# Kernel tuning notes

Hardware: AMD Instinct MI355X
Metric: run time of the kernel (lower is better)

## Reference

```python
import jax, jax.numpy as jnp
import numpy as np

B, S, D, H, E = 2, 2048, 1024, 4096, 8


def setup_inputs() -> dict:
    key = jax.random.key(0)
    k0, k1, k2, k3 = jax.random.split(key, 4)
    x = jax.random.normal(k0, (B, S, D), dtype=jnp.float32)
    router_w = jax.random.normal(k1, (E, D), dtype=jnp.float32) * 0.02   # Top2Router Linear weight [E, D]
    w1 = jax.random.normal(k2, (E, D, H), dtype=jnp.float32) * 0.02      # stacked fc1 weights (transposed: x @ w1[e])
    w2 = jax.random.normal(k3, (E, H, D), dtype=jnp.float32) * 0.02      # stacked fc2 weights
    return {"x": x, "router_w": router_w, "w1": w1, "w2": w2}


def reference(x, router_w, w1, w2):
    # x: [B, S, D] -> flatten tokens. Single-rank EP: all-to-all is identity,
    # microbatch split is a pure overlap trick, per-token math unchanged.
    b, s, d = x.shape
    e = router_w.shape[0]
    xf = x.reshape(-1, d)                                     # [T, D]
    # Top-2 router with renormalized gate weights
    probs = jax.nn.softmax(xf @ router_w.T, axis=-1)          # [T, E]
    topv, topi = jax.lax.top_k(probs, 2)                      # [T, 2]
    topv = topv / (topv.sum(axis=-1, keepdims=True) + 1e-9)
    # Combine weights per expert: cw[t,e] = sum_k topv[t,k] * [topi[t,k]==e]
    cw = (jax.nn.one_hot(topi, e, dtype=xf.dtype) * topv[..., None]).sum(axis=1)  # [T, E]
    # Expert MLPs (dense-over-experts reference for the grouped GEMM)
    h = jax.nn.gelu(jnp.einsum('td,edh->teh', xf, w1), approximate=False)  # [T, E, H]
    y = jnp.einsum('teh,ehd->ted', h, w2)                                   # [T, E, D]
    out = jnp.einsum('te,ted->td', cw, y)                                   # weighted combine (scatter-add equiv.)
    return out.reshape(b, s, d)
```

## Files before the change

### kernel.cpp

```cpp
#include <hip/hip_runtime.h>

#define T_TOK 4096
#define DIM   1024
#define HID   4096
#define NEXP  8
#define MAXROWS 9216

typedef unsigned short u16;
typedef __attribute__((ext_vector_type(8))) short short8;
typedef __attribute__((ext_vector_type(4))) float f32x4;
typedef __attribute__((ext_vector_type(4))) unsigned short u16x4;
typedef __attribute__((ext_vector_type(8))) unsigned short u16x8;

typedef __attribute__((address_space(3))) unsigned int lds_uint;
typedef const __attribute__((address_space(1))) unsigned int gbl_uint;

__device__ __forceinline__ u16 f2bf(float f) {
    union { float f; unsigned int u; } v; v.f = f;
    unsigned int r = v.u + 0x7fffu + ((v.u >> 16) & 1u);
    return (u16)(r >> 16);
}

__device__ __forceinline__ float gelu_f(float v) {
    float u = 1.5957691216f * (v + 0.044715f * v * v * v);
    float s = 1.0f / (1.0f + __expf(-u));
    return v * s;
}

__global__ __launch_bounds__(256)
void transpose_cast(const float* __restrict__ in, u16* __restrict__ out, int R, int C) {
    __shared__ u16 t[64 * 68];
    size_t mo = (size_t)blockIdx.z * R * C;
    const float* ip = in + mo;
    u16* op = out + mo;
    int c0 = blockIdx.x * 64, r0 = blockIdx.y * 64;
    int tid = threadIdx.x;
#pragma unroll
    for (int j = 0; j < 4; ++j) {
        int id = tid + 256 * j;
        int r = id >> 4, cc = id & 15;
        f32x4 v = *(const f32x4*)(ip + (size_t)(r0 + r) * C + c0 + 4 * cc);
        u16x4 w; w.x = f2bf(v.x); w.y = f2bf(v.y); w.z = f2bf(v.z); w.w = f2bf(v.w);
        *(u16x4*)(t + r * 68 + 4 * cc) = w;
    }
    __syncthreads();
#pragma unroll
    for (int j = 0; j < 4; ++j) {
        int id = tid + 256 * j;
        int c = id >> 4, rj = id & 15;
        u16x4 o;
        o.x = t[(4 * rj + 0) * 68 + c];
        o.y = t[(4 * rj + 1) * 68 + c];
        o.z = t[(4 * rj + 2) * 68 + c];
        o.w = t[(4 * rj + 3) * 68 + c];
        *(u16x4*)(op + (size_t)(c0 + c) * R + r0 + 4 * rj) = o;
    }
}

__global__ __launch_bounds__(256)
void router_k(const float* __restrict__ x, const float* __restrict__ rw,
              int* __restrict__ counts, int* __restrict__ tE,
              int* __restrict__ tS, float* __restrict__ tG) {
    int wave = threadIdx.x >> 6, lane = threadIdx.x & 63;
    int t = blockIdx.x * 4 + wave;
    const float* xr = x + (size_t)t * DIM;
    float xv[16];
#pragma unroll
    for (int i = 0; i < 16; ++i) xv[i] = xr[lane + 64*i];
    float lg[NEXP];
#pragma unroll
    for (int e = 0; e < NEXP; ++e) {
        const float* wr_ = rw + e * DIM;
        float a = 0.f;
#pragma unroll
        for (int i = 0; i < 16; ++i) a += xv[i] * wr_[lane + 64*i];
        lg[e] = a;
    }
#pragma unroll
    for (int off = 32; off > 0; off >>= 1)
#pragma unroll
        for (int e = 0; e < NEXP; ++e) lg[e] += __shfl_xor(lg[e], off, 64);
    if (lane == 0) {
        float mx = lg[0];
        for (int e = 1; e < NEXP; ++e) mx = fmaxf(mx, lg[e]);
        float p[NEXP], s = 0.f;
        for (int e = 0; e < NEXP; ++e) { p[e] = expf(lg[e] - mx); s += p[e]; }
        float inv_s = 1.f / s;
        for (int e = 0; e < NEXP; ++e) p[e] *= inv_s;
        int i0 = 0;
        for (int e = 1; e < NEXP; ++e) if (p[e] > p[i0]) i0 = e;
        int i1 = (i0 == 0) ? 1 : 0;
        for (int e = 0; e < NEXP; ++e) if (e != i0 && p[e] > p[i1]) i1 = e;
        float v0 = p[i0], v1 = p[i1];
        float inv = 1.f / (v0 + v1 + 1e-9f);
        int s0 = atomicAdd(&counts[i0], 1);
        int s1 = atomicAdd(&counts[i1], 1);
        tE[2*t] = i0;  tE[2*t+1] = i1;
        tS[2*t] = s0;  tS[2*t+1] = s1;
        tG[2*t] = v0 * inv;  tG[2*t+1] = v1 * inv;
    }
}

__global__ void scan_k(const int* __restrict__ counts, int* __restrict__ pbase) {
    if (threadIdx.x == 0) {
        int o = 0;
        for (int e = 0; e < NEXP; ++e) { pbase[e] = o; o += ((counts[e] + 127) >> 7) << 7; }
        pbase[NEXP] = o;
    }
}

__global__ __launch_bounds__(256)
void gather_k(const float* __restrict__ x, const int* __restrict__ tE,
              const int* __restrict__ tS, const int* __restrict__ pbase,
              u16* __restrict__ xg) {
    int a = blockIdx.x;
    int t = a >> 1, k = a & 1;
    int e = tE[2*t + k];
    int row = pbase[e] + tS[2*t + k];
    const f32x4* xr = (const f32x4*)(x + (size_t)t * DIM);
    u16x4* o = (u16x4*)(xg + (size_t)row * DIM);
    int i = threadIdx.x;
    f32x4 v = xr[i];
    u16x4 r; r.x = f2bf(v.x); r.y = f2bf(v.y); r.z = f2bf(v.z); r.w = f2bf(v.w);
    o[i] = r;
}

template<int K, int KSPLIT, bool GELU, typename OutT>
__global__ __launch_bounds__(256)
void gemm_bt(const u16* __restrict__ A, const u16* __restrict__ BtAll,
             OutT* __restrict__ C, const int* __restrict__ counts,
             const int* __restrict__ pbase, int N, size_t cstride) {
    int e  = blockIdx.z / KSPLIT;
    int ks = blockIdx.z % KSPLIT;
    int cnt = counts[e];
    int mt = blockIdx.y;
    if (mt * 128 >= cnt) return;
    const u16* Bt = BtAll + (size_t)e * N * K;
    OutT* Cp = C + (size_t)ks * cstride;
    int row0 = pbase[e] + mt * 128;
    int col0 = blockIdx.x * 128;
    const int kb0 = ks * (K / KSPLIT);
    const int kb1 = kb0 + (K / KSPLIT);

    __shared__ __align__(16) u16 smem[128 * 128];
    u16* As = smem;
    u16* Bs = smem + 128 * 64;

    int tid = threadIdx.x;
    int lane = tid & 63;
    int w = tid >> 6;
    int quad = lane >> 4, m16 = lane & 15;
    int wr = (w >> 1) * 64, wc = (w & 1) * 64;
    int rsub = lane >> 3;
    int kch  = lane & 7;

    f32x4 acc[4][4] = {};

    for (int kb = kb0; kb < kb1; kb += 64) {
#pragma unroll
        for (int i = 0; i < 4; ++i) {
            int grp = w * 4 + i;
            int r = grp * 8 + rsub;
            const u16* ga = A + (size_t)(row0 + r) * K + kb + kch * 8;
            __builtin_amdgcn_global_load_lds((gbl_uint*)ga, (lds_uint*)(As + grp * 512), 16, 0, 0);
            const u16* gb = Bt + (size_t)(col0 + r) * K + kb + kch * 8;
            __builtin_amdgcn_global_load_lds((gbl_uint*)gb, (lds_uint*)(Bs + grp * 512), 16, 0, 0);
        }
        __syncthreads();
#pragma unroll
        for (int ks2 = 0; ks2 < 64; ks2 += 32) {
            short8 af[4], bfr[4];
#pragma unroll
            for (int mi = 0; mi < 4; ++mi)
                af[mi] = *(const short8*)(As + (wr + mi * 16 + m16) * 64 + ks2 + quad * 8);
#pragma unroll
            for (int ni = 0; ni < 4; ++ni)
                bfr[ni] = *(const short8*)(Bs + (wc + ni * 16 + m16) * 64 + ks2 + quad * 8);
#pragma unroll
            for (int mi = 0; mi < 4; ++mi)
#pragma unroll
                for (int ni = 0; ni < 4; ++ni)
                    acc[mi][ni] = __builtin_amdgcn_mfma_f32_16x16x32_bf16(af[mi], bfr[ni], acc[mi][ni], 0, 0, 0);
        }
        __syncthreads();
    }

    if (GELU) {
#pragma unroll
        for (int mi = 0; mi < 4; ++mi) {
#pragma unroll
            for (int r = 0; r < 4; ++r) {
                int row = wr + mi * 16 + quad * 4 + r;
#pragma unroll
                for (int ni = 0; ni < 4; ++ni) {
                    int col = wc + ni * 16 + m16;
                    int c16 = col >> 3, w8 = col & 7;
                    smem[row * 128 + (((c16 ^ (row & 15)) << 3) | w8)] = f2bf(gelu_f(acc[mi][ni][r]));
                }
            }
        }
        __syncthreads();
#pragma unroll
        for (int j = 0; j < 8; ++j) {
            int id = tid + 256 * j;
            int row = id >> 4, c16 = id & 15;
            u16x8 val = *(const u16x8*)(smem + row * 128 + ((c16 ^ (row & 15)) << 3));
            *(u16x8*)((u16*)Cp + (size_t)(row0 + row) * N + col0 + c16 * 8) = val;
        }
    } else {
#pragma unroll
        for (int mi = 0; mi < 4; ++mi) {
#pragma unroll
            for (int r = 0; r < 4; ++r) {
                int mrow = wr + mi * 16 + quad * 4 + r;
                size_t rowoff = (size_t)(row0 + mrow) * N + col0;
#pragma unroll
                for (int ni = 0; ni < 4; ++ni) {
                    int ncol = wc + ni * 16 + m16;
                    ((float*)Cp)[rowoff + ncol] = acc[mi][ni][r];
                }
            }
        }
    }
}

__global__ __launch_bounds__(256)
void combine_k(const float* __restrict__ p0, const float* __restrict__ p1,
               const int* __restrict__ tE, const int* __restrict__ tS,
               const float* __restrict__ tG, const int* __restrict__ pbase,
               float* __restrict__ out) {
    int t = blockIdx.x;
    int e0 = tE[2*t], e1 = tE[2*t+1];
    int r0 = pbase[e0] + tS[2*t];
    int r1 = pbase[e1] + tS[2*t+1];
    float g0 = tG[2*t], g1 = tG[2*t+1];
    int i = threadIdx.x;
    f32x4 a0 = ((const f32x4*)(p0 + (size_t)r0 * DIM))[i];
    f32x4 b0 = ((const f32x4*)(p1 + (size_t)r0 * DIM))[i];
    f32x4 a1 = ((const f32x4*)(p0 + (size_t)r1 * DIM))[i];
    f32x4 b1 = ((const f32x4*)(p1 + (size_t)r1 * DIM))[i];
    f32x4* o = (f32x4*)(out + (size_t)t * DIM);
    o[i] = g0 * (a0 + b0) + g1 * (a1 + b1);
}

extern "C" void kernel_launch(void* const* d_in, const int* in_sizes, int n_in,
                              void* d_out, int out_size, void* d_ws, size_t ws_size,
                              hipStream_t stream) {
    const float* x  = (const float*)d_in[0];
    const float* rw = (const float*)d_in[1];
    const float* w1 = (const float*)d_in[2];
    const float* w2 = (const float*)d_in[3];
    float* out = (float*)d_out;

    char* ws = (char*)d_ws;
    u16* w1t = (u16*)(ws + 0);
    u16* xg  = (u16*)(ws + 67108864ull);
    u16* w2t = (u16*)(ws + 85983232ull);
    u16* hb  = (u16*)(ws + 153092096ull);
    float* p0 = (float*)(ws + 0);
    float* p1 = (float*)(ws + 37748736ull);
    int* ctrl   = (int*)(ws + 228589568ull);
    int* counts = ctrl;
    int* pbase  = ctrl + 8;
    int* tE     = ctrl + 32;
    int* tS     = ctrl + 32 + 8192;
    float* tG   = (float*)(ctrl + 32 + 16384);

    hipMemsetAsync(counts, 0, 8 * sizeof(int), stream);

    transpose_cast<<<dim3(HID / 64, DIM / 64, NEXP), 256, 0, stream>>>(w1, w1t, DIM, HID);
    transpose_cast<<<dim3(DIM / 64, HID / 64, NEXP), 256, 0, stream>>>(w2, w2t, HID, DIM);
    router_k<<<T_TOK / 4, 256, 0, stream>>>(x, rw, counts, tE, tS, tG);
    scan_k<<<1, 64, 0, stream>>>(counts, pbase);
    gather_k<<<T_TOK * 2, 256, 0, stream>>>(x, tE, tS, pbase, xg);
    gemm_bt<DIM, 1, true, u16><<<dim3(HID / 128, 32, NEXP), 256, 0, stream>>>(
        xg, w1t, hb, counts, pbase, HID, 0);
    gemm_bt<HID, 2, false, float><<<dim3(DIM / 128, 32, NEXP * 2), 256, 0, stream>>>(
        hb, w2t, p0, counts, pbase, DIM, (size_t)MAXROWS * DIM);
    combine_k<<<T_TOK, 256, 0, stream>>>(p0, p1, tE, tS, tG, pbase, out);
}
```

Measured before the change: 735.9 us.

## Merge weight transposes, drop scan and memset, swizzle GEMM LDS loads

The two weight transpose-cast launches become one kernel that also zeroes the expert counts, which removes the memset. The scan kernel is dropped, and each consumer recomputes expert base offsets inline from the counts. The GEMM now XOR-swizzles the LDS layout to avoid bank conflicts, keeps precomputed pointers that advance each K step, and simplifies epilogue addressing. This trims launch overhead and LDS conflicts at the cost of a little redundant offset arithmetic per block.

```diff
diff --git a/kernel.cpp b/kernel.cpp
--- a/kernel.cpp
+++ b/kernel.cpp
@@ -28,12 +28,25 @@
 }
 
 __global__ __launch_bounds__(256)
-void transpose_cast(const float* __restrict__ in, u16* __restrict__ out, int R, int C) {
+void transpose_cast2(const float* __restrict__ w1, u16* __restrict__ w1t,
+                     const float* __restrict__ w2, u16* __restrict__ w2t,
+                     int* __restrict__ counts) {
+    int b = blockIdx.x;
+    if (b == 0 && threadIdx.x < NEXP) counts[threadIdx.x] = 0;
+    const float* in; u16* out; int R, C, bx, by, e;
+    if (b < 8192) {
+        e = b >> 10; int t = b & 1023; bx = t & 63; by = t >> 6;
+        in = w1; out = w1t; R = DIM; C = HID;
+    } else {
+        b -= 8192;
+        e = b >> 10; int t = b & 1023; bx = t & 15; by = t >> 4;
+        in = w2; out = w2t; R = HID; C = DIM;
+    }
     __shared__ u16 t[64 * 68];
-    size_t mo = (size_t)blockIdx.z * R * C;
+    size_t mo = (size_t)e * DIM * HID;
     const float* ip = in + mo;
     u16* op = out + mo;
-    int c0 = blockIdx.x * 64, r0 = blockIdx.y * 64;
+    int c0 = bx * 64, r0 = by * 64;
     int tid = threadIdx.x;
 #pragma unroll
     for (int j = 0; j < 4; ++j) {
@@ -101,22 +114,24 @@
     }
 }
 
-__global__ void scan_k(const int* __restrict__ counts, int* __restrict__ pbase) {
-    if (threadIdx.x == 0) {
-        int o = 0;
-        for (int e = 0; e < NEXP; ++e) { pbase[e] = o; o += ((counts[e] + 127) >> 7) << 7; }
-        pbase[NEXP] = o;
-    }
+__device__ __forceinline__ int pbase_of(const int* __restrict__ counts, int e) {
+    int pb = 0;
+#pragma unroll
+    for (int i = 0; i < NEXP; ++i) {
+        int pad = ((counts[i] + 127) >> 7) << 7;
+        pb += (i < e) ? pad : 0;
+    }
+    return pb;
 }
 
 __global__ __launch_bounds__(256)
 void gather_k(const float* __restrict__ x, const int* __restrict__ tE,
-              const int* __restrict__ tS, const int* __restrict__ pbase,
+              const int* __restrict__ tS, const int* __restrict__ counts,
               u16* __restrict__ xg) {
     int a = blockIdx.x;
     int t = a >> 1, k = a & 1;
     int e = tE[2*t + k];
-    int row = pbase[e] + tS[2*t + k];
+    int row = pbase_of(counts, e) + tS[2*t + k];
     const f32x4* xr = (const f32x4*)(x + (size_t)t * DIM);
     u16x4* o = (u16x4*)(xg + (size_t)row * DIM);
     int i = threadIdx.x;
@@ -129,18 +144,18 @@
 __global__ __launch_bounds__(256)
 void gemm_bt(const u16* __restrict__ A, const u16* __restrict__ BtAll,
              OutT* __restrict__ C, const int* __restrict__ counts,
-             const int* __restrict__ pbase, int N, size_t cstride) {
+             int N, size_t cstride) {
     int e  = blockIdx.z / KSPLIT;
     int ks = blockIdx.z % KSPLIT;
     int cnt = counts[e];
     int mt = blockIdx.y;
     if (mt * 128 >= cnt) return;
+    int row0 = pbase_of(counts, e) + mt * 128;
     const u16* Bt = BtAll + (size_t)e * N * K;
     OutT* Cp = C + (size_t)ks * cstride;
-    int row0 = pbase[e] + mt * 128;
     int col0 = blockIdx.x * 128;
     const int kb0 = ks * (K / KSPLIT);
-    const int kb1 = kb0 + (K / KSPLIT);
+    constexpr int KITER = K / KSPLIT / 64;
 
     __shared__ __align__(16) u16 smem[128 * 128];
     u16* As = smem;
@@ -153,29 +168,48 @@
     int wr = (w >> 1) * 64, wc = (w & 1) * 64;
     int rsub = lane >> 3;
     int kch  = lane & 7;
+    int kchs = kch ^ rsub;
+
+    const u16* ga[4];
+    const u16* gb[4];
+#pragma unroll
+    for (int i = 0; i < 4; ++i) {
+        int r = (w * 4 + i) * 8 + rsub;
+        ga[i] = A  + (size_t)(row0 + r) * K + kb0 + kchs * 8;
+        gb[i] = Bt + (size_t)(col0 + r) * K + kb0 + kchs * 8;
+    }
+    int sw = m16 & 7;
+    const u16* aP0 = As + (wr + m16) * 64 + ((quad       ^ sw) << 3);
+    const u16* aP1 = As + (wr + m16) * 64 + (((4 + quad) ^ sw) << 3);
+    const u16* bP0 = Bs + (wc + m16) * 64 + ((quad       ^ sw) << 3);
+    const u16* bP1 = Bs + (wc + m16) * 64 + (((4 + quad) ^ sw) << 3);
 
     f32x4 acc[4][4] = {};
 
-    for (int kb = kb0; kb < kb1; kb += 64) {
+    for (int kit = 0; kit < KITER; ++kit) {
 #pragma unroll
         for (int i = 0; i < 4; ++i) {
             int grp = w * 4 + i;
-            int r = grp * 8 + rsub;
-            const u16* ga = A + (size_t)(row0 + r) * K + kb + kch * 8;
-            __builtin_amdgcn_global_load_lds((gbl_uint*)ga, (lds_uint*)(As + grp * 512), 16, 0, 0);
-            const u16* gb = Bt + (size_t)(col0 + r) * K + kb + kch * 8;
-            __builtin_amdgcn_global_load_lds((gbl_uint*)gb, (lds_uint*)(Bs + grp * 512), 16, 0, 0);
+            __builtin_amdgcn_global_load_lds((gbl_uint*)ga[i], (lds_uint*)(As + grp * 512), 16, 0, 0);
+            __builtin_amdgcn_global_load_lds((gbl_uint*)gb[i], (lds_uint*)(Bs + grp * 512), 16, 0, 0);
+            ga[i] += 64; gb[i] += 64;
         }
         __syncthreads();
-#pragma unroll
-        for (int ks2 = 0; ks2 < 64; ks2 += 32) {
+        {
             short8 af[4], bfr[4];
 #pragma unroll
+            for (int mi = 0; mi < 4; ++mi) af[mi]  = *(const short8*)(aP0 + mi * 1024);
+#pragma unroll
+            for (int ni = 0; ni < 4; ++ni) bfr[ni] = *(const short8*)(bP0 + ni * 1024);
+#pragma unroll
             for (int mi = 0; mi < 4; ++mi)
-                af[mi] = *(const short8*)(As + (wr + mi * 16 + m16) * 64 + ks2 + quad * 8);
-#pragma unroll
-            for (int ni = 0; ni < 4; ++ni)
-                bfr[ni] = *(const short8*)(Bs + (wc + ni * 16 + m16) * 64 + ks2 + quad * 8);
+#pragma unroll
+                for (int ni = 0; ni < 4; ++ni)
+                    acc[mi][ni] = __builtin_amdgcn_mfma_f32_16x16x32_bf16(af[mi], bfr[ni], acc[mi][ni], 0, 0, 0);
+#pragma unroll
+            for (int mi = 0; mi < 4; ++mi) af[mi]  = *(const short8*)(aP1 + mi * 1024);
+#pragma unroll
+            for (int ni = 0; ni < 4; ++ni) bfr[ni] = *(const short8*)(bP1 + ni * 1024);
 #pragma unroll
             for (int mi = 0; mi < 4; ++mi)
 #pragma unroll
@@ -200,39 +234,38 @@
             }
         }
         __syncthreads();
+        int row_b = tid >> 4, c16_b = tid & 15;
+        const u16* ls = smem + row_b * 128 + (((c16_b ^ (row_b & 15)) << 3));
+        u16* gp = (u16*)Cp + (size_t)(row0 + row_b) * N + col0 + c16_b * 8;
 #pragma unroll
         for (int j = 0; j < 8; ++j) {
-            int id = tid + 256 * j;
-            int row = id >> 4, c16 = id & 15;
-            u16x8 val = *(const u16x8*)(smem + row * 128 + ((c16 ^ (row & 15)) << 3));
-            *(u16x8*)((u16*)Cp + (size_t)(row0 + row) * N + col0 + c16 * 8) = val;
+            *(u16x8*)gp = *(const u16x8*)ls;
+            ls += 16 * 128;
+            gp += (size_t)16 * N;
         }
     } else {
-#pragma unroll
-        for (int mi = 0; mi < 4; ++mi) {
+        float* gp = (float*)Cp + (size_t)(row0 + wr + quad * 4) * N + col0 + wc + m16;
+#pragma unroll
+        for (int mi = 0; mi < 4; ++mi)
 #pragma unroll
             for (int r = 0; r < 4; ++r) {
-                int mrow = wr + mi * 16 + quad * 4 + r;
-                size_t rowoff = (size_t)(row0 + mrow) * N + col0;
-#pragma unroll
-                for (int ni = 0; ni < 4; ++ni) {
-                    int ncol = wc + ni * 16 + m16;
-                    ((float*)Cp)[rowoff + ncol] = acc[mi][ni][r];
-                }
+                float* rp = gp + (size_t)(mi * 16 + r) * N;
+#pragma unroll
+                for (int ni = 0; ni < 4; ++ni)
+                    rp[ni * 16] = acc[mi][ni][r];
             }
-        }
     }
 }
 
 __global__ __launch_bounds__(256)
 void combine_k(const float* __restrict__ p0, const float* __restrict__ p1,
                const int* __restrict__ tE, const int* __restrict__ tS,
-               const float* __restrict__ tG, const int* __restrict__ pbase,
+               const float* __restrict__ tG, const int* __restrict__ counts,
                float* __restrict__ out) {
     int t = blockIdx.x;
     int e0 = tE[2*t], e1 = tE[2*t+1];
-    int r0 = pbase[e0] + tS[2*t];
-    int r1 = pbase[e1] + tS[2*t+1];
+    int r0 = pbase_of(counts, e0) + tS[2*t];
+    int r1 = pbase_of(counts, e1) + tS[2*t+1];
     float g0 = tG[2*t], g1 = tG[2*t+1];
     int i = threadIdx.x;
     f32x4 a0 = ((const f32x4*)(p0 + (size_t)r0 * DIM))[i];
@@ -261,21 +294,16 @@
     float* p1 = (float*)(ws + 37748736ull);
     int* ctrl   = (int*)(ws + 228589568ull);
     int* counts = ctrl;
-    int* pbase  = ctrl + 8;
     int* tE     = ctrl + 32;
     int* tS     = ctrl + 32 + 8192;
     float* tG   = (float*)(ctrl + 32 + 16384);
 
-    hipMemsetAsync(counts, 0, 8 * sizeof(int), stream);
-
-    transpose_cast<<<dim3(HID / 64, DIM / 64, NEXP), 256, 0, stream>>>(w1, w1t, DIM, HID);
-    transpose_cast<<<dim3(DIM / 64, HID / 64, NEXP), 256, 0, stream>>>(w2, w2t, HID, DIM);
+    transpose_cast2<<<16384, 256, 0, stream>>>(w1, w1t, w2, w2t, counts);
     router_k<<<T_TOK / 4, 256, 0, stream>>>(x, rw, counts, tE, tS, tG);
-    scan_k<<<1, 64, 0, stream>>>(counts, pbase);
-    gather_k<<<T_TOK * 2, 256, 0, stream>>>(x, tE, tS, pbase, xg);
+    gather_k<<<T_TOK * 2, 256, 0, stream>>>(x, tE, tS, counts, xg);
     gemm_bt<DIM, 1, true, u16><<<dim3(HID / 128, 32, NEXP), 256, 0, stream>>>(
-        xg, w1t, hb, counts, pbase, HID, 0);
+        xg, w1t, hb, counts, HID, 0);
     gemm_bt<HID, 2, false, float><<<dim3(DIM / 128, 32, NEXP * 2), 256, 0, stream>>>(
-        hb, w2t, p0, counts, pbase, DIM, (size_t)MAXROWS * DIM);
-    combine_k<<<T_TOK, 256, 0, stream>>>(p0, p1, tE, tS, tG, pbase, out);
-}
+        hb, w2t, p0, counts, DIM, (size_t)MAXROWS * DIM);
+    combine_k<<<T_TOK, 256, 0, stream>>>(p0, p1, tE, tS, tG, counts, out);
+}
```

After: 671.8 us. -8.7%, faster.
